# Performance work log

Hardware: AMD Instinct MI355X
Metric: run time of the kernel (lower is better)

## Reference

```python
import jax, jax.numpy as jnp
import numpy as np

K = -1.0          # manifold curvature (hyperbolic / Poincare ball)
EPS = 1e-15

def _artanh(x):
    return jnp.arctanh(jnp.clip(x, -1.0 + 1e-7, 1.0 - 1e-7))

def _norm(x, keepdims=True):
    return jnp.sqrt(jnp.maximum(jnp.sum(x * x, axis=-1, keepdims=keepdims), EPS * EPS))

def expmap0(u):
    # sqrt(-K) == 1 for K = -1
    un = _norm(u)
    return jnp.tanh(un) * u / un

def logmap0(x):
    xn = _norm(x)
    return _artanh(xn) * x / xn

def mobius_matvec(m, x):
    xn = _norm(x)
    mx = x @ m
    mxn = _norm(mx)
    return jnp.tanh(mxn / xn * _artanh(xn)) * mx / mxn

def mobius_scalar_mul(r, x):
    xn = _norm(x)
    return jnp.tanh(r * _artanh(xn)) * x / xn

def mobius_add(x, y):
    x2 = jnp.sum(x * x, -1, keepdims=True)
    y2 = jnp.sum(y * y, -1, keepdims=True)
    xy = jnp.sum(x * y, -1, keepdims=True)
    num = (1.0 - 2.0 * K * xy - K * y2) * x + (1.0 + K * x2) * y
    den = 1.0 - 2.0 * K * xy + K * K * x2 * y2
    return num / jnp.maximum(den, EPS)

def lambda_x(x, keepdims=True):
    x2 = jnp.sum(x * x, -1, keepdims=keepdims)
    return 2.0 / jnp.maximum(1.0 + K * x2, EPS)

def kappa_layer(X, A, W):
    # mobius matvec + adjacency-weighted gyromidpoint (lincomb=True) + sigma
    XW = mobius_matvec(W, X)                       # [N, D]
    gamma = lambda_x(XW)                           # [N, 1] conformal factor
    denom = A @ (gamma - 1.0)                      # [N, 1]
    nom = A @ (gamma * XW)                         # [N, D]
    denom = jnp.where(denom >= 0, jnp.maximum(denom, 1e-10), jnp.minimum(denom, -1e-10))
    a_mean = mobius_scalar_mul(0.5, nom / denom)   # gyromidpoint
    alpha = jnp.sum(A, axis=1, keepdims=True)      # lincomb scaling
    AXW = mobius_scalar_mul(alpha, a_mean)
    return expmap0(jax.nn.relu(logmap0(AXW)))      # sigma = exp(relu(log(x)))

def get_logits(X, W, b):
    z = mobius_add(-b[None, :, :], X[:, None, :])              # [N, C, D]
    zn = jnp.maximum(_norm(z, keepdims=False), 1e-10)          # [N, C]
    an = jnp.maximum(jnp.linalg.norm(W, axis=0), 1e-10)        # [C]
    za = jnp.einsum('ncd,dc->nc', z, W)                        # [N, C]
    dist = jnp.arcsinh(2.0 * za / ((1.0 + K * zn ** 2) * an))  # arsin_k, kappa*|kappa| = -1
    lam_b = lambda_x(b, keepdims=False)                        # [C]
    return (lam_b * an) * dist

def _forward(X, A_hat, W1, W2, W_logits, p_ks):
    X = kappa_layer(X, A_hat, W1)
    X = kappa_layer(X, A_hat, W2)
    logits = get_logits(X, W_logits, p_ks)
    return A_hat @ logits                          # aggregate_logits=True


def setup_inputs() -> dict:
    key = jax.random.key(0)
    ks = jax.random.split(key, 6)
    N, D, C = 8192, 32, 16
    # node features are points on the manifold: expmap0 of small tangent vectors
    X = expmap0(jax.random.normal(ks[0], (N, D), jnp.float32) * 0.1)
    # dense non-negative normalized-adjacency-like weights, row sums ~ 1.5
    A_hat = jax.random.uniform(ks[1], (N, N), dtype=jnp.float32) * (3.0 / N)
    W1 = jax.random.normal(ks[2], (D, D), jnp.float32) * 0.01
    W2 = jax.random.normal(ks[3], (D, D), jnp.float32) * 0.01
    W_logits = jax.random.normal(ks[4], (D, C), jnp.float32) * 0.01
    p_ks = expmap0(jax.random.normal(ks[5], (C, D), jnp.float32) * 0.01)
    return {"X": X, "A_hat": A_hat, "W1": W1, "W2": W2,
            "W_logits": W_logits, "p_ks": p_ks}


def reference(X, A_hat, W1, W2, W_logits, p_ks):
    return _forward(X, A_hat, W1, W2, W_logits, p_ks)
```

## Files before the change

kernel.cpp:

```cpp
#include <hip/hip_runtime.h>

#define N_NODES 8192
#define DIM 32
#define NCLS 16
#define SPLITK 16
#define KSEG (N_NODES / SPLITK)
#define NCOLC 36
#define NKT (N_NODES / 32)
#define RT_STRIDE ((size_t)NKT * 512)
#define PITCH 520

typedef __bf16 bf16x8 __attribute__((ext_vector_type(8)));
typedef float f32x4 __attribute__((ext_vector_type(4)));

__device__ inline unsigned short f2bf(float f) {
  unsigned u = __float_as_uint(f);
  u = u + 0x7FFFu + ((u >> 16) & 1u);
  return (unsigned short)(u >> 16);
}

__device__ inline float artanh_pos(float x) {
  x = fminf(x, 1.0f - 1e-7f);
  return 0.5f * logf((1.0f + x) / (1.0f - x));
}

__device__ inline size_t a_tile_idx(int r, int k) {
  return ((size_t)(r >> 4) * NKT + (k >> 5)) * 512 + (size_t)((r & 15) * 32 + (k & 31));
}
__device__ inline size_t g_tile_idx(int c, int n) {
  return ((size_t)(n >> 5) * 3 + (c >> 4)) * 512 + (size_t)((c & 15) * 32 + (n & 31));
}
__device__ inline size_t l_tile_idx(int c, int n) {
  return (size_t)(n >> 5) * 512 + (size_t)(c * 32 + (n & 31));
}

__global__ __launch_bounds__(256) void k_convert(const float* __restrict__ A,
                                                 unsigned short* __restrict__ Abf) {
  __shared__ unsigned short lds[16 * PITCH];
  const int t = threadIdx.x;
  const int NST = (N_NODES / 16) * (N_NODES / 512);
  for (int st = blockIdx.x; st < NST; st += gridDim.x) {
    const int rt = st >> 4;
    const int ks = st & 15;
    const float* src = A + (size_t)(rt * 16) * N_NODES + ks * 512;
#pragma unroll
    for (int v = 0; v < 8; v++) {
      const int row = 2 * v + (t >> 7);
      const int k = (t & 127) * 4;
      float4 f = *(const float4*)(src + (size_t)row * N_NODES + k);
      uint2 o;
      o.x = f2bf(f.x) | ((unsigned)f2bf(f.y) << 16);
      o.y = f2bf(f.z) | ((unsigned)f2bf(f.w) << 16);
      *(uint2*)(lds + row * PITCH + k) = o;
    }
    __syncthreads();
    unsigned short* dst = Abf + (size_t)st * 8192;
#pragma unroll
    for (int u = 0; u < 4; u++) {
      const int p = u * 256 + t;
      const int kt = p >> 6;
      const int q = p & 63;
      const int row = q >> 2;
      const int kl = (q & 3) * 8;
      bf16x8 val = *(const bf16x8*)(lds + row * PITCH + kt * 32 + kl);
      *(bf16x8*)(dst + (size_t)p * 8) = val;
    }
    __syncthreads();
  }
}

__device__ inline void pre_math(const float* __restrict__ Wl, const float x[DIM],
                                unsigned short* __restrict__ GT, int n) {
  float xn2 = 0.f;
#pragma unroll
  for (int i = 0; i < DIM; i++) xn2 += x[i] * x[i];
  float xn = sqrtf(fmaxf(xn2, 1e-30f));
  float mx[DIM];
#pragma unroll
  for (int j = 0; j < DIM; j++) mx[j] = 0.f;
  for (int i = 0; i < DIM; i++) {
    float xi = x[i];
#pragma unroll
    for (int j = 0; j < DIM; j++) mx[j] = fmaf(xi, Wl[i * DIM + j], mx[j]);
  }
  float mxn2 = 0.f;
#pragma unroll
  for (int j = 0; j < DIM; j++) mxn2 += mx[j] * mx[j];
  float mxn = sqrtf(fmaxf(mxn2, 1e-30f));
  float t = tanhf(mxn / xn * artanh_pos(xn));
  float sc = t / mxn;
  float xw[DIM];
  float x2n = 0.f;
#pragma unroll
  for (int j = 0; j < DIM; j++) { xw[j] = sc * mx[j]; x2n += xw[j] * xw[j]; }
  float gamma = 2.0f / fmaxf(1.0f - x2n, 1e-15f);
#pragma unroll
  for (int c = 0; c < DIM; c++) GT[g_tile_idx(c, n)] = f2bf(gamma * xw[c]);
  GT[g_tile_idx(32, n)] = f2bf(gamma - 1.0f);
  GT[g_tile_idx(33, n)] = f2bf(1.0f);
#pragma unroll
  for (int c = DIM + 2; c < 48; c++) GT[g_tile_idx(c, n)] = 0;
}

__global__ void k_pre1(const float* __restrict__ X, const float* __restrict__ W,
                       unsigned short* __restrict__ GT) {
  __shared__ float Wl[DIM * DIM];
  for (int i = threadIdx.x; i < DIM * DIM; i += blockDim.x) Wl[i] = W[i];
  __syncthreads();
  const int n = blockIdx.x * blockDim.x + threadIdx.x;
  float x[DIM];
#pragma unroll
  for (int i = 0; i < DIM; i += 4) {
    float4 v = *(const float4*)(X + (size_t)n * DIM + i);
    x[i] = v.x; x[i + 1] = v.y; x[i + 2] = v.z; x[i + 3] = v.w;
  }
  pre_math(Wl, x, GT, n);
}

__device__ inline void post_math(const float* __restrict__ Cred, int n, float xo[DIM]) {
  float acc[36];
  const float4* p = (const float4*)(Cred + (size_t)n * NCOLC);
#pragma unroll
  for (int q = 0; q < 9; q++) {
    float4 v = p[q];
    acc[q * 4 + 0] = v.x; acc[q * 4 + 1] = v.y;
    acc[q * 4 + 2] = v.z; acc[q * 4 + 3] = v.w;
  }
  float denom = acc[32];
  float alpha = acc[33];
  denom = (denom >= 0.f) ? fmaxf(denom, 1e-10f) : fminf(denom, -1e-10f);
  float inv = 1.0f / denom;
  float v[DIM];
  float vn2 = 0.f;
#pragma unroll
  for (int c = 0; c < DIM; c++) { v[c] = acc[c] * inv; vn2 += v[c] * v[c]; }
  float vn = sqrtf(fmaxf(vn2, 1e-30f));
  float un = alpha * 0.5f * artanh_pos(vn);
  float su = un / vn;
  float r[DIM];
  float rn2 = 0.f;
#pragma unroll
  for (int c = 0; c < DIM; c++) { r[c] = fmaxf(su * v[c], 0.f); rn2 += r[c] * r[c]; }
  float rn = sqrtf(fmaxf(rn2, 1e-30f));
  float so = tanhf(rn) / rn;
#pragma unroll
  for (int c = 0; c < DIM; c++) xo[c] = so * r[c];
}

__global__ void k_postpre(const float* __restrict__ Cred, const float* __restrict__ W,
                          unsigned short* __restrict__ GT) {
  __shared__ float Wl[DIM * DIM];
  for (int i = threadIdx.x; i < DIM * DIM; i += blockDim.x) Wl[i] = W[i];
  __syncthreads();
  const int n = blockIdx.x * blockDim.x + threadIdx.x;
  float x[DIM];
  post_math(Cred, n, x);
  pre_math(Wl, x, GT, n);
}

__global__ void k_postlogits(const float* __restrict__ Cred, const float* __restrict__ Wl_g,
                             const float* __restrict__ B_g, unsigned short* __restrict__ LT) {
  __shared__ float Wc[DIM * NCLS];
  __shared__ float Bc[NCLS * DIM];
  __shared__ float an_s[NCLS], lam_s[NCLS], b2_s[NCLS];
  for (int i = threadIdx.x; i < DIM * NCLS; i += blockDim.x) { Wc[i] = Wl_g[i]; Bc[i] = B_g[i]; }
  __syncthreads();
  if (threadIdx.x < NCLS) {
    int c = threadIdx.x;
    float b2 = 0.f, w2 = 0.f;
    for (int d = 0; d < DIM; d++) {
      b2 += Bc[c * DIM + d] * Bc[c * DIM + d];
      w2 += Wc[d * NCLS + c] * Wc[d * NCLS + c];
    }
    b2_s[c] = b2;
    an_s[c] = fmaxf(sqrtf(w2), 1e-10f);
    lam_s[c] = 2.0f / fmaxf(1.0f - b2, 1e-15f);
  }
  __syncthreads();
  const int n = blockIdx.x * blockDim.x + threadIdx.x;
  float x[DIM];
  post_math(Cred, n, x);
  float y2 = 0.f;
#pragma unroll
  for (int i = 0; i < DIM; i++) y2 += x[i] * x[i];
  for (int c = 0; c < NCLS; c++) {
    float b2 = b2_s[c];
    float bx = 0.f;
    for (int d = 0; d < DIM; d++) bx += Bc[c * DIM + d] * x[d];
    float xy = -bx;
    float f1 = 1.0f + 2.0f * xy + y2;
    float f2 = 1.0f - b2;
    float den = fmaxf(1.0f + 2.0f * xy + b2 * y2, 1e-15f);
    float invden = 1.0f / den;
    float zn2 = 0.f, za = 0.f;
    for (int d = 0; d < DIM; d++) {
      float z = (f1 * (-Bc[c * DIM + d]) + f2 * x[d]) * invden;
      zn2 += z * z;
      za += z * Wc[d * NCLS + c];
    }
    float zn = fmaxf(sqrtf(fmaxf(zn2, 1e-30f)), 1e-10f);
    float dist = asinhf(2.0f * za / ((1.0f - zn * zn) * an_s[c]));
    LT[l_tile_idx(c, n)] = f2bf(lam_s[c] * an_s[c] * dist);
  }
}

template <int NF>
__global__ __launch_bounds__(256) void k_mm(const unsigned short* __restrict__ A,
                                            const unsigned short* __restrict__ BT,
                                            float* __restrict__ Cpart) {
  const int lane = threadIdx.x & 63;
  const int wid = threadIdx.x >> 6;
  const int r0 = blockIdx.x * 128 + wid * 32;
  const int kt0 = blockIdx.y * (KSEG / 32);
  const int lr = lane & 15;
  const int lkg = lane >> 4;
  const int poff = lr * 32 + lkg * 8;
  const int BS = (NF == 3) ? 3 : 1;
  f32x4 acc[2][NF];
#pragma unroll
  for (int m = 0; m < 2; m++)
#pragma unroll
    for (int nf = 0; nf < NF; nf++) acc[m][nf] = (f32x4){0.f, 0.f, 0.f, 0.f};
  const unsigned short* pa0 = A + ((size_t)(r0 >> 4) * NKT + kt0) * 512 + poff;
  const unsigned short* pa1 = pa0 + RT_STRIDE;
  const unsigned short* pbB = BT + (size_t)kt0 * BS * 512 + poff;
#pragma unroll 4
  for (int kt = 0; kt < KSEG / 32; kt++) {
    bf16x8 a0 = *(const bf16x8*)(pa0 + (size_t)kt * 512);
    bf16x8 a1 = *(const bf16x8*)(pa1 + (size_t)kt * 512);
#pragma unroll
    for (int nf = 0; nf < NF; nf++) {
      bf16x8 b = *(const bf16x8*)(pbB + (size_t)(kt * BS + nf) * 512);
      acc[0][nf] = __builtin_amdgcn_mfma_f32_16x16x32_bf16(a0, b, acc[0][nf], 0, 0, 0);
      acc[1][nf] = __builtin_amdgcn_mfma_f32_16x16x32_bf16(a1, b, acc[1][nf], 0, 0, 0);
    }
  }
  const int NCOL = (NF == 3) ? NCOLC : NF * 16;
  float* Cb = Cpart + (size_t)blockIdx.y * N_NODES * NCOL;
#pragma unroll
  for (int m = 0; m < 2; m++)
#pragma unroll
    for (int nf = 0; nf < NF; nf++) {
      if (NF == 3 && nf == 2 && lr >= 4) continue;
#pragma unroll
      for (int j = 0; j < 4; j++) {
        int row = r0 + m * 16 + lkg * 4 + j;
        int col = nf * 16 + lr;
        Cb[(size_t)row * NCOL + col] = acc[m][nf][j];
      }
    }
}

template <int TOTAL>
__global__ void k_red(const float* __restrict__ part, float* __restrict__ outb) {
  int i = blockIdx.x * blockDim.x + threadIdx.x;
  if (i < TOTAL) {
    float s = 0.f;
#pragma unroll
    for (int q = 0; q < SPLITK; q++) s += part[(size_t)q * TOTAL + i];
    outb[i] = s;
  }
}

extern "C" void kernel_launch(void* const* d_in, const int* in_sizes, int n_in,
                              void* d_out, int out_size, void* d_ws, size_t ws_size,
                              hipStream_t stream) {
  (void)in_sizes; (void)n_in; (void)out_size; (void)ws_size;
  const float* X  = (const float*)d_in[0];
  const float* A  = (const float*)d_in[1];
  const float* W1 = (const float*)d_in[2];
  const float* W2 = (const float*)d_in[3];
  const float* WL = (const float*)d_in[4];
  const float* PK = (const float*)d_in[5];
  float* out = (float*)d_out;

  char* ws = (char*)d_ws;
  unsigned short* Abf = (unsigned short*)ws;
  unsigned short* GT  = (unsigned short*)(ws + 134217728);
  float* Cpart        = (float*)(ws + 135004160);
  float* Cred         = (float*)(ws + 153878528);
  unsigned short* LT  = (unsigned short*)(ws + 155058176);

  k_convert<<<2048, 256, 0, stream>>>(A, Abf);

  k_pre1<<<N_NODES / 64, 64, 0, stream>>>(X, W1, GT);
  k_mm<3><<<dim3(64, SPLITK), 256, 0, stream>>>(Abf, GT, Cpart);
  k_red<N_NODES * NCOLC><<<N_NODES * NCOLC / 256, 256, 0, stream>>>(Cpart, Cred);
  k_postpre<<<N_NODES / 64, 64, 0, stream>>>(Cred, W2, GT);

  k_mm<3><<<dim3(64, SPLITK), 256, 0, stream>>>(Abf, GT, Cpart);
  k_red<N_NODES * NCOLC><<<N_NODES * NCOLC / 256, 256, 0, stream>>>(Cpart, Cred);
  k_postlogits<<<N_NODES / 64, 64, 0, stream>>>(Cred, WL, PK, LT);

  k_mm<1><<<dim3(64, SPLITK), 256, 0, stream>>>(Abf, LT, Cpart);
  k_red<N_NODES * NCLS><<<N_NODES * NCLS / 256, 256, 0, stream>>>(Cpart, out);
}
```

Measured before the change: 212.6 us.

## Fuse fp32-to-bf16 adjacency conversion into first split-K matmul

```diff
diff --git a/kernel.cpp b/kernel.cpp
--- a/kernel.cpp
+++ b/kernel.cpp
@@ -24,9 +24,6 @@
   return 0.5f * logf((1.0f + x) / (1.0f - x));
 }
 
-__device__ inline size_t a_tile_idx(int r, int k) {
-  return ((size_t)(r >> 4) * NKT + (k >> 5)) * 512 + (size_t)((r & 15) * 32 + (k & 31));
-}
 __device__ inline size_t g_tile_idx(int c, int n) {
   return ((size_t)(n >> 5) * 3 + (c >> 4)) * 512 + (size_t)((c & 15) * 32 + (n & 31));
 }
@@ -34,38 +31,76 @@
   return (size_t)(n >> 5) * 512 + (size_t)(c * 32 + (n & 31));
 }
 
-__global__ __launch_bounds__(256) void k_convert(const float* __restrict__ A,
-                                                 unsigned short* __restrict__ Abf) {
-  __shared__ unsigned short lds[16 * PITCH];
+__global__ __launch_bounds__(256) void k_mmc(const float* __restrict__ A,
+                                             const unsigned short* __restrict__ GT,
+                                             unsigned short* __restrict__ Abf,
+                                             float* __restrict__ Cpart) {
+  __shared__ __align__(16) unsigned char ldsraw[16 * PITCH * 2];
+  unsigned short* lds_t = (unsigned short*)ldsraw;
+  float* lds_r = (float*)ldsraw;
   const int t = threadIdx.x;
-  const int NST = (N_NODES / 16) * (N_NODES / 512);
-  for (int st = blockIdx.x; st < NST; st += gridDim.x) {
-    const int rt = st >> 4;
-    const int ks = st & 15;
-    const float* src = A + (size_t)(rt * 16) * N_NODES + ks * 512;
-#pragma unroll
-    for (int v = 0; v < 8; v++) {
-      const int row = 2 * v + (t >> 7);
-      const int k = (t & 127) * 4;
-      float4 f = *(const float4*)(src + (size_t)row * N_NODES + k);
-      uint2 o;
-      o.x = f2bf(f.x) | ((unsigned)f2bf(f.y) << 16);
-      o.y = f2bf(f.z) | ((unsigned)f2bf(f.w) << 16);
-      *(uint2*)(lds + row * PITCH + k) = o;
-    }
-    __syncthreads();
-    unsigned short* dst = Abf + (size_t)st * 8192;
-#pragma unroll
-    for (int u = 0; u < 4; u++) {
-      const int p = u * 256 + t;
-      const int kt = p >> 6;
-      const int q = p & 63;
-      const int row = q >> 2;
-      const int kl = (q & 3) * 8;
-      bf16x8 val = *(const bf16x8*)(lds + row * PITCH + kt * 32 + kl);
-      *(bf16x8*)(dst + (size_t)p * 8) = val;
-    }
-    __syncthreads();
+  const int st = blockIdx.x;
+  const int rt = st >> 4;
+  const int ks = st & 15;
+  const int lane = t & 63;
+  const int w = t >> 6;
+  const int lr = lane & 15;
+  const int lkg = lane >> 4;
+
+  const float* src = A + (size_t)(rt * 16) * N_NODES + ks * 512;
+#pragma unroll
+  for (int v = 0; v < 8; v++) {
+    const int row = 2 * v + (t >> 7);
+    const int k = (t & 127) * 4;
+    float4 f = *(const float4*)(src + (size_t)row * N_NODES + k);
+    uint2 o;
+    o.x = f2bf(f.x) | ((unsigned)f2bf(f.y) << 16);
+    o.y = f2bf(f.z) | ((unsigned)f2bf(f.w) << 16);
+    *(uint2*)(lds_t + row * PITCH + k) = o;
+  }
+  __syncthreads();
+
+  f32x4 acc[3];
+#pragma unroll
+  for (int nf = 0; nf < 3; nf++) acc[nf] = (f32x4){0.f, 0.f, 0.f, 0.f};
+  const int poff = lr * 32 + lkg * 8;
+#pragma unroll
+  for (int i = 0; i < 4; i++) {
+    const int kt2 = 4 * w + i;
+    bf16x8 a = *(const bf16x8*)(lds_t + lr * PITCH + kt2 * 32 + lkg * 8);
+#pragma unroll
+    for (int nf = 0; nf < 3; nf++) {
+      bf16x8 b = *(const bf16x8*)(GT + ((size_t)(ks * 16 + kt2) * 3 + nf) * 512 + poff);
+      acc[nf] = __builtin_amdgcn_mfma_f32_16x16x32_bf16(a, b, acc[nf], 0, 0, 0);
+    }
+  }
+
+  unsigned short* dst = Abf + (size_t)st * 8192;
+#pragma unroll
+  for (int u = 0; u < 4; u++) {
+    const int p = u * 256 + t;
+    const int kt = p >> 6;
+    const int q = p & 63;
+    const int row = q >> 2;
+    const int kl = (q & 3) * 8;
+    bf16x8 val = *(const bf16x8*)(lds_t + row * PITCH + kt * 32 + kl);
+    *(bf16x8*)(dst + (size_t)p * 8) = val;
+  }
+  __syncthreads();
+
+#pragma unroll
+  for (int nf = 0; nf < 3; nf++)
+#pragma unroll
+    for (int j = 0; j < 4; j++)
+      lds_r[(w * 16 + lkg * 4 + j) * 48 + nf * 16 + lr] = acc[nf][j];
+  __syncthreads();
+
+  for (int e = t; e < 16 * 36; e += 256) {
+    const int row = e / 36;
+    const int col = e % 36;
+    float s = lds_r[row * 48 + col] + lds_r[768 + row * 48 + col] +
+              lds_r[1536 + row * 48 + col] + lds_r[2304 + row * 48 + col];
+    Cpart[((size_t)ks * N_NODES + rt * 16 + row) * NCOLC + col] = s;
   }
 }
 
@@ -281,10 +316,8 @@
   float* Cred         = (float*)(ws + 153878528);
   unsigned short* LT  = (unsigned short*)(ws + 155058176);
 
-  k_convert<<<2048, 256, 0, stream>>>(A, Abf);
-
   k_pre1<<<N_NODES / 64, 64, 0, stream>>>(X, W1, GT);
-  k_mm<3><<<dim3(64, SPLITK), 256, 0, stream>>>(Abf, GT, Cpart);
+  k_mmc<<<8192, 256, 0, stream>>>(A, GT, Abf, Cpart);
   k_red<N_NODES * NCOLC><<<N_NODES * NCOLC / 256, 256, 0, stream>>>(Cpart, Cred);
   k_postpre<<<N_NODES / 64, 64, 0, stream>>>(Cred, W2, GT);
 
```

Result: faster. 190.7 us (-10.3%).
